# Performance work log

Measured on AMD Instinct MI355X. Metric: run time of the kernel, lower is better.

Reference implementation:

```python
import jax, jax.numpy as jnp
import numpy as np

B, D, L = 16384, 1024, 4


def setup_inputs() -> dict:
    key = jax.random.key(0)
    ks = jax.random.split(key, 5)
    scale = 1.0 / np.sqrt(D)
    x = jax.random.normal(ks[0], (B, D), dtype=jnp.float32)
    # torch nn.Linear default init: U(-1/sqrt(fan_in), 1/sqrt(fan_in))
    Ws = jax.random.uniform(ks[1], (L, D, D), jnp.float32, -scale, scale)
    bs = jax.random.uniform(ks[2], (L, D), jnp.float32, -scale, scale)
    Wo = jax.random.uniform(ks[3], (D, D), jnp.float32, -scale, scale)
    bo = jax.random.uniform(ks[4], (D,), jnp.float32, -scale, scale)
    return {"x": x, "Ws": Ws, "bs": bs, "Wo": Wo, "bo": bo}


def reference(x, Ws, bs, Wo, bo):
    # torch: matmul(x[:, :, None], x[:, None, :]).sum(2) == x * x.sum(-1, keepdims=True)
    interactions = jax.nn.relu(x * jnp.sum(x, axis=-1, keepdims=True))  # (B, D)
    h = x
    for i in range(L):  # fixed small layer count
        h = jax.nn.relu(h @ Ws[i].T + bs[i])  # torch Linear: y = x W^T + b
    out = ((h + interactions) * 0.5) @ Wo.T + bo
    return out
```

## Files before the change

kernel.cpp:

```cpp
#include <hip/hip_runtime.h>


#define DDIM 1024
#define BROWS 16384
#define NIT 8

typedef __attribute__((ext_vector_type(8))) short s8v;
typedef __attribute__((ext_vector_type(4))) float f4v;

__device__ __forceinline__ unsigned short f2bf(float f) {
    unsigned int u = __float_as_uint(f);
    u += 0x7fffu + ((u >> 16) & 1u);
    return (unsigned short)(u >> 16);
}
__device__ __forceinline__ float bf2f(unsigned short u) {
    return __uint_as_float(((unsigned int)u) << 16);
}
__device__ __forceinline__ void gld16(const void* g, void* l) {
    __builtin_amdgcn_global_load_lds(
        (const __attribute__((address_space(1))) unsigned int*)g,
        (__attribute__((address_space(3))) unsigned int*)l, 16, 0, 0);
}

__global__ __launch_bounds__(256) void prep_cvt_kernel(
    const float* __restrict__ x,  const float* __restrict__ Ws,
    const float* __restrict__ Wo, unsigned short* __restrict__ xb,
    unsigned short* __restrict__ wb, float* __restrict__ rowsum)
{
    const int t = threadIdx.x;
    if (blockIdx.x < BROWS) {
        const int row = blockIdx.x;
        const float4 v = *(const float4*)(x + (size_t)row * DDIM + t * 4);
        ushort4 o;
        o.x = f2bf(v.x); o.y = f2bf(v.y); o.z = f2bf(v.z); o.w = f2bf(v.w);
        *(ushort4*)(xb + (size_t)row * DDIM + t * 4) = o;
        float s = v.x + v.y + v.z + v.w;
        #pragma unroll
        for (int off = 32; off > 0; off >>= 1) s += __shfl_down(s, off, 64);
        __shared__ float red[4];
        const int wave = t >> 6, lane = t & 63;
        if (lane == 0) red[wave] = s;
        __syncthreads();
        if (t == 0) rowsum[row] = red[0] + red[1] + red[2] + red[3];
    } else {
        const int base = (blockIdx.x - BROWS) * 1024;
        #pragma unroll
        for (int j = 0; j < 4; ++j) {
            const int idx = base + j * 256 + t;
            const float4 v = (idx < 4 * 262144) ? ((const float4*)Ws)[idx]
                                                : ((const float4*)Wo)[idx - 4 * 262144];
            ushort4 o;
            o.x = f2bf(v.x); o.y = f2bf(v.y); o.z = f2bf(v.z); o.w = f2bf(v.w);
            ((ushort4*)wb)[idx] = o;
        }
    }
}

#define MF(a, b, c) __builtin_amdgcn_mfma_f32_16x16x32_bf16(a, b, c, 0, 0, 0)
#define BAR()   __builtin_amdgcn_s_barrier()
#define VMC(n)  asm volatile("s_waitcnt vmcnt(" #n ")" ::: "memory")

#define SWOFF(lr, cc) ((lr) * 128 + ((((cc) ^ ((lr) & 7))) << 4))

#define SH(src, dst) {                                              \
    gld16((src) + soff,                   (char*)(dst) + t * 16);   \
    gld16((src) + soff + (size_t)64 * K,  (char*)(dst) + t * 16 + 8192); }

#define READ_A(P, m0) {                                                               \
    af[0][0] = *(const s8v*)((const char*)(P) + SWOFF((m0) * 16 + mrow,      quad));      \
    af[0][1] = *(const s8v*)((const char*)(P) + SWOFF((m0) * 16 + mrow,      4 + quad));  \
    af[1][0] = *(const s8v*)((const char*)(P) + SWOFF((m0) * 16 + 16 + mrow, quad));      \
    af[1][1] = *(const s8v*)((const char*)(P) + SWOFF((m0) * 16 + 16 + mrow, 4 + quad)); }

#define READ_B(P) {                                                                   \
    bfr[0][0] = *(const s8v*)((const char*)(P) + SWOFF(bl + mrow,      quad));            \
    bfr[0][1] = *(const s8v*)((const char*)(P) + SWOFF(bl + mrow,      4 + quad));        \
    bfr[1][0] = *(const s8v*)((const char*)(P) + SWOFF(bl + 16 + mrow, quad));            \
    bfr[1][1] = *(const s8v*)((const char*)(P) + SWOFF(bl + 16 + mrow, 4 + quad));        \
    bfr[2][0] = *(const s8v*)((const char*)(P) + SWOFF(bl + 32 + mrow, quad));            \
    bfr[2][1] = *(const s8v*)((const char*)(P) + SWOFF(bl + 32 + mrow, 4 + quad));        \
    bfr[3][0] = *(const s8v*)((const char*)(P) + SWOFF(bl + 48 + mrow, quad));            \
    bfr[3][1] = *(const s8v*)((const char*)(P) + SWOFF(bl + 48 + mrow, 4 + quad)); }

#define MMA8(m0, s) {                                              \
    acc[m0][0]       = MF(af[0][s], bfr[0][s], acc[m0][0]);        \
    acc[m0][1]       = MF(af[0][s], bfr[1][s], acc[m0][1]);        \
    acc[m0][2]       = MF(af[0][s], bfr[2][s], acc[m0][2]);        \
    acc[m0][3]       = MF(af[0][s], bfr[3][s], acc[m0][3]);        \
    acc[(m0) + 1][0] = MF(af[1][s], bfr[0][s], acc[(m0) + 1][0]);  \
    acc[(m0) + 1][1] = MF(af[1][s], bfr[1][s], acc[(m0) + 1][1]);  \
    acc[(m0) + 1][2] = MF(af[1][s], bfr[2][s], acc[(m0) + 1][2]);  \
    acc[(m0) + 1][3] = MF(af[1][s], bfr[3][s], acc[(m0) + 1][3]); }

#define MMA16(m0) { __builtin_amdgcn_s_setprio(1); MMA8(m0, 0) MMA8(m0, 1) \
                    __builtin_amdgcn_s_setprio(0); }

template <int MODE>
__global__ __launch_bounds__(512, 2) void gemm256(
    const unsigned short* __restrict__ A,
    const unsigned short* __restrict__ Bw,
    const float* __restrict__ bias,
    void* __restrict__ out,
    const unsigned short* __restrict__ xb,
    const float* __restrict__ rowsum)
{
    constexpr int K = DDIM, N = DDIM;
    __shared__ unsigned short smem[2][2][2][128 * 64];

    const int t = threadIdx.x;
    const int lane = t & 63;
    const int wid  = t >> 6;
    const int wr   = wid >> 2;
    const int wc   = wid & 3;
    const int mrow = lane & 15;
    const int quad = lane >> 4;
    const int rowBase = blockIdx.x * 256;
    const int colBase = blockIdx.y * 256;

    const unsigned short* const Ab0 = A  + (size_t)rowBase * K;
    const unsigned short* const Ab1 = Ab0 + (size_t)128 * K;
    const unsigned short* const Bb0 = Bw + (size_t)colBase * K;
    const unsigned short* const Bb1 = Bb0 + (size_t)128 * K;

    const int srow = t >> 3;
    const size_t soff = (size_t)srow * K + (size_t)(((t & 7) ^ (srow & 7)) * 8);

    unsigned short* const a00 = &smem[0][0][0][0];
    unsigned short* const a01 = &smem[0][0][1][0];
    unsigned short* const a10 = &smem[0][1][0][0];
    unsigned short* const a11 = &smem[0][1][1][0];
    unsigned short* const b00 = &smem[1][0][0][0];
    unsigned short* const b01 = &smem[1][0][1][0];
    unsigned short* const b10 = &smem[1][1][0][0];
    unsigned short* const b11 = &smem[1][1][1][0];

    const unsigned short* const aR0 = wr ? a01 : a00;
    const unsigned short* const aR1 = wr ? a11 : a10;
    const unsigned short* const bR0 = (wc >> 1) ? b01 : b00;
    const unsigned short* const bR1 = (wc >> 1) ? b11 : b10;
    const int bl = (wc & 1) * 64;

    f4v acc[8][4] = {};
    s8v af[2][2], bfr[4][2];

    SH(Ab0,      a00); SH(Ab1,      a01);
    SH(Bb0,      b00); SH(Bb1,      b01);
    SH(Bb0 + 64, b10); SH(Bb1 + 64, b11);
    VMC(4);
    BAR();
    READ_B(bR0); READ_A(aR0, 0);

    #pragma unroll 1
    for (int it = 0; it < NIT; ++it) {
        const int ka = it * 128, kb = ka + 64;
        const bool more = it < NIT - 1;

        SH(Ab0 + kb, a10);
        BAR(); MMA16(0); BAR();
        READ_A(aR0, 2);
        SH(Ab1 + kb, a11);
        BAR(); MMA16(2); BAR();
        READ_A(aR0, 4);
        if (more) SH(Bb0 + ka + 128, b00);
        BAR(); MMA16(4); BAR();
        READ_A(aR0, 6);
        if (more) SH(Bb1 + ka + 128, b01);
        if (more) { VMC(4); } else { VMC(0); }
        BAR();
        MMA16(6);
        READ_B(bR1); READ_A(aR1, 0);
        BAR();

        if (more) SH(Ab0 + ka + 128, a00);
        BAR(); MMA16(0); BAR();
        READ_A(aR1, 2);
        if (more) SH(Ab1 + ka + 128, a01);
        BAR(); MMA16(2); BAR();
        READ_A(aR1, 4);
        if (more) SH(Bb0 + kb + 128, b10);
        BAR(); MMA16(4); BAR();
        READ_A(aR1, 6);
        if (more) SH(Bb1 + kb + 128, b11);
        if (more) { VMC(4); }
        BAR();
        MMA16(6);
        if (more) { READ_B(bR0); READ_A(aR0, 0); }
        BAR();
    }

    if (MODE == 2) {
        float* sCf = (float*)smem;
        float* o = (float*)out;
        #pragma unroll 1
        for (int half = 0; half < 2; ++half) {
            __syncthreads();
            if (wr == half) {
                #pragma unroll
                for (int ni = 0; ni < 4; ++ni) {
                    const int n = wc * 64 + ni * 16 + mrow;
                    const float bv = bias[colBase + n];
                    #pragma unroll
                    for (int mi = 0; mi < 8; ++mi)
                        #pragma unroll
                        for (int r = 0; r < 4; ++r)
                            sCf[(mi * 16 + quad * 4 + r) * 256 + n] = acc[mi][ni][r] + bv;
                }
            }
            __syncthreads();
            #pragma unroll
            for (int p = 0; p < 16; ++p) {
                const int idx = t + p * 512;
                const int row = idx >> 6, ch = idx & 63;
                const float4 v = ((const float4*)sCf)[idx];
                *(float4*)(o + (size_t)(rowBase + half * 128 + row) * N + colBase + ch * 4) = v;
            }
        }
    } else {
        __syncthreads();
        unsigned short* sC = (unsigned short*)smem;
        #pragma unroll
        for (int ni = 0; ni < 4; ++ni) {
            const int n = wc * 64 + ni * 16 + mrow;
            const float bv = bias[colBase + n];
            #pragma unroll
            for (int mi = 0; mi < 8; ++mi)
                #pragma unroll
                for (int r = 0; r < 4; ++r) {
                    const int row = wr * 128 + mi * 16 + quad * 4 + r;
                    float v = acc[mi][ni][r] + bv;
                    v = v > 0.f ? v : 0.f;
                    sC[row * 256 + n] = f2bf(v);
                }
        }
        __syncthreads();
        unsigned short* o16 = (unsigned short*)out;
        #pragma unroll
        for (int p = 0; p < 16; ++p) {
            const int idx = t + p * 512;
            const int row = idx >> 5, ch = idx & 31;
            s8v c = *(const s8v*)&sC[row * 256 + ch * 8];
            if (MODE == 1) {
                const float rsv = rowsum[rowBase + row];
                const s8v xv = *(const s8v*)&xb[(size_t)(rowBase + row) * DDIM + colBase + ch * 8];
                #pragma unroll
                for (int j = 0; j < 8; ++j) {
                    float itv = bf2f((unsigned short)xv[j]) * rsv;
                    itv = itv > 0.f ? itv : 0.f;
                    c[j] = (short)f2bf(0.5f * (bf2f((unsigned short)c[j]) + itv));
                }
            }
            *(s8v*)&o16[(size_t)(rowBase + row) * DDIM + colBase + ch * 8] = c;
        }
    }
}

extern "C" void kernel_launch(void* const* d_in, const int* in_sizes, int n_in,
                              void* d_out, int out_size, void* d_ws, size_t ws_size,
                              hipStream_t stream) {
    const float* x  = (const float*)d_in[0];
    const float* Ws = (const float*)d_in[1];
    const float* bs = (const float*)d_in[2];
    const float* Wo = (const float*)d_in[3];
    const float* bo = (const float*)d_in[4];
    float* out = (float*)d_out;

    char* ws = (char*)d_ws;
    unsigned short* xb  = (unsigned short*)(ws);
    unsigned short* h0  = (unsigned short*)(ws + 33554432);
    unsigned short* h1  = (unsigned short*)(ws + 67108864);
    unsigned short* wb  = (unsigned short*)(ws + 100663296);
    float*          rsm = (float*)(ws + 111149056);

    prep_cvt_kernel<<<BROWS + 1280, 256, 0, stream>>>(x, Ws, Wo, xb, wb, rsm);

    const size_t WSZ = (size_t)DDIM * DDIM;
    dim3 g(BROWS / 256, DDIM / 256);
    gemm256<0><<<g, 512, 0, stream>>>(xb, wb,           bs,            h0, nullptr, nullptr);
    gemm256<0><<<g, 512, 0, stream>>>(h0, wb + 1 * WSZ, bs + 1 * DDIM, h1, nullptr, nullptr);
    gemm256<0><<<g, 512, 0, stream>>>(h1, wb + 2 * WSZ, bs + 2 * DDIM, h0, nullptr, nullptr);
    gemm256<1><<<g, 512, 0, stream>>>(h0, wb + 3 * WSZ, bs + 3 * DDIM, h1, xb, rsm);
    gemm256<2><<<g, 512, 0, stream>>>(h1, wb + 4 * WSZ, bo,            out, nullptr, nullptr);
}
```

Measured before the change: 317.7 us.

## Fuse prep and all five GEMM layers into one cooperative persistent kernel

Replaces the conversion kernel and the five per-layer GEMM launches with a single cooperative kernel whose 256 blocks each cover one output tile per layer. The input/weight conversion and row sums now run inside it, and grid-wide syncs with thread fences separate the phases. The goal is to remove the launch gaps and tail effects between six kernels. In exchange, every layer waits for the slowest block at a grid barrier, and the cooperative launch requires all 256 blocks to be resident at once (two per CU).

```diff
diff --git a/kernel.cpp b/kernel.cpp
--- a/kernel.cpp
+++ b/kernel.cpp
@@ -1,4 +1,7 @@
 #include <hip/hip_runtime.h>
+#include <hip/hip_cooperative_groups.h>
+
+namespace cg = cooperative_groups;
 
 
 #define DDIM 1024
@@ -20,40 +23,6 @@
     __builtin_amdgcn_global_load_lds(
         (const __attribute__((address_space(1))) unsigned int*)g,
         (__attribute__((address_space(3))) unsigned int*)l, 16, 0, 0);
-}
-
-__global__ __launch_bounds__(256) void prep_cvt_kernel(
-    const float* __restrict__ x,  const float* __restrict__ Ws,
-    const float* __restrict__ Wo, unsigned short* __restrict__ xb,
-    unsigned short* __restrict__ wb, float* __restrict__ rowsum)
-{
-    const int t = threadIdx.x;
-    if (blockIdx.x < BROWS) {
-        const int row = blockIdx.x;
-        const float4 v = *(const float4*)(x + (size_t)row * DDIM + t * 4);
-        ushort4 o;
-        o.x = f2bf(v.x); o.y = f2bf(v.y); o.z = f2bf(v.z); o.w = f2bf(v.w);
-        *(ushort4*)(xb + (size_t)row * DDIM + t * 4) = o;
-        float s = v.x + v.y + v.z + v.w;
-        #pragma unroll
-        for (int off = 32; off > 0; off >>= 1) s += __shfl_down(s, off, 64);
-        __shared__ float red[4];
-        const int wave = t >> 6, lane = t & 63;
-        if (lane == 0) red[wave] = s;
-        __syncthreads();
-        if (t == 0) rowsum[row] = red[0] + red[1] + red[2] + red[3];
-    } else {
-        const int base = (blockIdx.x - BROWS) * 1024;
-        #pragma unroll
-        for (int j = 0; j < 4; ++j) {
-            const int idx = base + j * 256 + t;
-            const float4 v = (idx < 4 * 262144) ? ((const float4*)Ws)[idx]
-                                                : ((const float4*)Wo)[idx - 4 * 262144];
-            ushort4 o;
-            o.x = f2bf(v.x); o.y = f2bf(v.y); o.z = f2bf(v.z); o.w = f2bf(v.w);
-            ((ushort4*)wb)[idx] = o;
-        }
-    }
 }
 
 #define MF(a, b, c) __builtin_amdgcn_mfma_f32_16x16x32_bf16(a, b, c, 0, 0, 0)
@@ -95,17 +64,18 @@
 #define MMA16(m0) { __builtin_amdgcn_s_setprio(1); MMA8(m0, 0) MMA8(m0, 1) \
                     __builtin_amdgcn_s_setprio(0); }
 
-template <int MODE>
-__global__ __launch_bounds__(512, 2) void gemm256(
-    const unsigned short* __restrict__ A,
-    const unsigned short* __restrict__ Bw,
-    const float* __restrict__ bias,
-    void* __restrict__ out,
-    const unsigned short* __restrict__ xb,
-    const float* __restrict__ rowsum)
+__global__ __launch_bounds__(512, 2) void deepfm_fused(
+    const float* __restrict__ x,  const float* __restrict__ Ws,
+    const float* __restrict__ bs, const float* __restrict__ Wo,
+    const float* __restrict__ bo, float* __restrict__ out,
+    unsigned short* __restrict__ xb, unsigned short* __restrict__ h0,
+    unsigned short* __restrict__ h1, unsigned short* __restrict__ wb,
+    float* __restrict__ rsm)
 {
     constexpr int K = DDIM, N = DDIM;
     __shared__ unsigned short smem[2][2][2][128 * 64];
+
+    cg::grid_group grid = cg::this_grid();
 
     const int t = threadIdx.x;
     const int lane = t & 63;
@@ -116,11 +86,40 @@
     const int quad = lane >> 4;
     const int rowBase = blockIdx.x * 256;
     const int colBase = blockIdx.y * 256;
-
-    const unsigned short* const Ab0 = A  + (size_t)rowBase * K;
-    const unsigned short* const Ab1 = Ab0 + (size_t)128 * K;
-    const unsigned short* const Bb0 = Bw + (size_t)colBase * K;
-    const unsigned short* const Bb1 = Bb0 + (size_t)128 * K;
+    const int bid = blockIdx.x * 4 + blockIdx.y;
+
+    {
+        const int rbase = bid * 64;
+        #pragma unroll 1
+        for (int g = 0; g < 8; ++g) {
+            const int row = rbase + g * 8 + wid;
+            const float* xr = x + (size_t)row * DDIM;
+            float s = 0.f;
+            #pragma unroll
+            for (int j = 0; j < 4; ++j) {
+                const float4 v = *(const float4*)(xr + (j * 64 + lane) * 4);
+                ushort4 o;
+                o.x = f2bf(v.x); o.y = f2bf(v.y); o.z = f2bf(v.z); o.w = f2bf(v.w);
+                *(ushort4*)(xb + (size_t)row * DDIM + (j * 64 + lane) * 4) = o;
+                s += v.x + v.y + v.z + v.w;
+            }
+            #pragma unroll
+            for (int off = 32; off > 0; off >>= 1) s += __shfl_down(s, off, 64);
+            if (lane == 0) rsm[row] = s;
+        }
+        #pragma unroll
+        for (int j = 0; j < 10; ++j) {
+            const int idx = bid * 5120 + j * 512 + t;
+            const float4 v = (idx < 4 * 262144) ? ((const float4*)Ws)[idx]
+                                                : ((const float4*)Wo)[idx - 4 * 262144];
+            ushort4 o;
+            o.x = f2bf(v.x); o.y = f2bf(v.y); o.z = f2bf(v.z); o.w = f2bf(v.w);
+            ((ushort4*)wb)[idx] = o;
+        }
+    }
+    __threadfence();
+    grid.sync();
+    __threadfence();
 
     const int srow = t >> 3;
     const size_t soff = (size_t)srow * K + (size_t)(((t & 7) ^ (srow & 7)) * 8);
@@ -140,116 +139,133 @@
     const unsigned short* const bR1 = (wc >> 1) ? b11 : b10;
     const int bl = (wc & 1) * 64;
 
-    f4v acc[8][4] = {};
-    s8v af[2][2], bfr[4][2];
-
-    SH(Ab0,      a00); SH(Ab1,      a01);
-    SH(Bb0,      b00); SH(Bb1,      b01);
-    SH(Bb0 + 64, b10); SH(Bb1 + 64, b11);
-    VMC(4);
-    BAR();
-    READ_B(bR0); READ_A(aR0, 0);
-
     #pragma unroll 1
-    for (int it = 0; it < NIT; ++it) {
-        const int ka = it * 128, kb = ka + 64;
-        const bool more = it < NIT - 1;
-
-        SH(Ab0 + kb, a10);
-        BAR(); MMA16(0); BAR();
-        READ_A(aR0, 2);
-        SH(Ab1 + kb, a11);
-        BAR(); MMA16(2); BAR();
-        READ_A(aR0, 4);
-        if (more) SH(Bb0 + ka + 128, b00);
-        BAR(); MMA16(4); BAR();
-        READ_A(aR0, 6);
-        if (more) SH(Bb1 + ka + 128, b01);
-        if (more) { VMC(4); } else { VMC(0); }
+    for (int l = 0; l < 5; ++l) {
+        const unsigned short* Acur = (l == 0) ? xb : ((l & 1) ? h0 : h1);
+        const unsigned short* Bwc  = wb + (size_t)l * DDIM * DDIM;
+        const float* bias = (l == 4) ? bo : (bs + (size_t)l * DDIM);
+        unsigned short* outb = (l & 1) ? h1 : h0;
+
+        const unsigned short* const Ab0 = Acur + (size_t)rowBase * K;
+        const unsigned short* const Ab1 = Ab0 + (size_t)128 * K;
+        const unsigned short* const Bb0 = Bwc + (size_t)colBase * K;
+        const unsigned short* const Bb1 = Bb0 + (size_t)128 * K;
+
+        f4v acc[8][4] = {};
+        s8v af[2][2], bfr[4][2];
+
+        SH(Ab0,      a00); SH(Ab1,      a01);
+        SH(Bb0,      b00); SH(Bb1,      b01);
+        SH(Bb0 + 64, b10); SH(Bb1 + 64, b11);
+        VMC(4);
         BAR();
-        MMA16(6);
-        READ_B(bR1); READ_A(aR1, 0);
-        BAR();
-
-        if (more) SH(Ab0 + ka + 128, a00);
-        BAR(); MMA16(0); BAR();
-        READ_A(aR1, 2);
-        if (more) SH(Ab1 + ka + 128, a01);
-        BAR(); MMA16(2); BAR();
-        READ_A(aR1, 4);
-        if (more) SH(Bb0 + kb + 128, b10);
-        BAR(); MMA16(4); BAR();
-        READ_A(aR1, 6);
-        if (more) SH(Bb1 + kb + 128, b11);
-        if (more) { VMC(4); }
-        BAR();
-        MMA16(6);
-        if (more) { READ_B(bR0); READ_A(aR0, 0); }
-        BAR();
-    }
-
-    if (MODE == 2) {
-        float* sCf = (float*)smem;
-        float* o = (float*)out;
+        READ_B(bR0); READ_A(aR0, 0);
+
         #pragma unroll 1
-        for (int half = 0; half < 2; ++half) {
+        for (int it = 0; it < NIT; ++it) {
+            const int ka = it * 128, kb = ka + 64;
+            const bool more = it < NIT - 1;
+
+            SH(Ab0 + kb, a10);
+            BAR(); MMA16(0); BAR();
+            READ_A(aR0, 2);
+            SH(Ab1 + kb, a11);
+            BAR(); MMA16(2); BAR();
+            READ_A(aR0, 4);
+            if (more) SH(Bb0 + ka + 128, b00);
+            BAR(); MMA16(4); BAR();
+            READ_A(aR0, 6);
+            if (more) SH(Bb1 + ka + 128, b01);
+            if (more) { VMC(4); } else { VMC(0); }
+            BAR();
+            MMA16(6);
+            READ_B(bR1); READ_A(aR1, 0);
+            BAR();
+
+            if (more) SH(Ab0 + ka + 128, a00);
+            BAR(); MMA16(0); BAR();
+            READ_A(aR1, 2);
+            if (more) SH(Ab1 + ka + 128, a01);
+            BAR(); MMA16(2); BAR();
+            READ_A(aR1, 4);
+            if (more) SH(Bb0 + kb + 128, b10);
+            BAR(); MMA16(4); BAR();
+            READ_A(aR1, 6);
+            if (more) SH(Bb1 + kb + 128, b11);
+            if (more) { VMC(4); }
+            BAR();
+            MMA16(6);
+            if (more) { READ_B(bR0); READ_A(aR0, 0); }
+            BAR();
+        }
+
+        if (l == 4) {
+            float* sCf = (float*)smem;
+            #pragma unroll 1
+            for (int half = 0; half < 2; ++half) {
+                __syncthreads();
+                if (wr == half) {
+                    #pragma unroll
+                    for (int ni = 0; ni < 4; ++ni) {
+                        const int n = wc * 64 + ni * 16 + mrow;
+                        const float bv = bias[colBase + n];
+                        #pragma unroll
+                        for (int mi = 0; mi < 8; ++mi)
+                            #pragma unroll
+                            for (int r = 0; r < 4; ++r)
+                                sCf[(mi * 16 + quad * 4 + r) * 256 + n] = acc[mi][ni][r] + bv;
+                    }
+                }
+                __syncthreads();
+                #pragma unroll
+                for (int p = 0; p < 16; ++p) {
+                    const int idx = t + p * 512;
+                    const int row = idx >> 6, ch = idx & 63;
+                    const float4 v = ((const float4*)sCf)[idx];
+                    *(float4*)(out + (size_t)(rowBase + half * 128 + row) * N + colBase + ch * 4) = v;
+                }
+            }
+        } else {
             __syncthreads();
-            if (wr == half) {
+            unsigned short* sC = (unsigned short*)smem;
+            #pragma unroll
+            for (int ni = 0; ni < 4; ++ni) {
+                const int n = wc * 64 + ni * 16 + mrow;
+                const float bv = bias[colBase + n];
                 #pragma unroll
-                for (int ni = 0; ni < 4; ++ni) {
-                    const int n = wc * 64 + ni * 16 + mrow;
-                    const float bv = bias[colBase + n];
+                for (int mi = 0; mi < 8; ++mi)
                     #pragma unroll
-                    for (int mi = 0; mi < 8; ++mi)
-                        #pragma unroll
-                        for (int r = 0; r < 4; ++r)
-                            sCf[(mi * 16 + quad * 4 + r) * 256 + n] = acc[mi][ni][r] + bv;
-                }
+                    for (int r = 0; r < 4; ++r) {
+                        const int row = wr * 128 + mi * 16 + quad * 4 + r;
+                        float v = acc[mi][ni][r] + bv;
+                        v = v > 0.f ? v : 0.f;
+                        sC[row * 256 + n] = f2bf(v);
+                    }
             }
             __syncthreads();
             #pragma unroll
             for (int p = 0; p < 16; ++p) {
                 const int idx = t + p * 512;
-                const int row = idx >> 6, ch = idx & 63;
-                const float4 v = ((const float4*)sCf)[idx];
-                *(float4*)(o + (size_t)(rowBase + half * 128 + row) * N + colBase + ch * 4) = v;
-            }
-        }
-    } else {
-        __syncthreads();
-        unsigned short* sC = (unsigned short*)smem;
-        #pragma unroll
-        for (int ni = 0; ni < 4; ++ni) {
-            const int n = wc * 64 + ni * 16 + mrow;
-            const float bv = bias[colBase + n];
-            #pragma unroll
-            for (int mi = 0; mi < 8; ++mi)
-                #pragma unroll
-                for (int r = 0; r < 4; ++r) {
-                    const int row = wr * 128 + mi * 16 + quad * 4 + r;
-                    float v = acc[mi][ni][r] + bv;
-                    v = v > 0.f ? v : 0.f;
-                    sC[row * 256 + n] = f2bf(v);
+                const int row = idx >> 5, ch = idx & 31;
+                s8v c = *(const s8v*)&sC[row * 256 + ch * 8];
+                if (l == 3) {
+                    const float rsv = rsm[rowBase + row];
+                    const s8v xv = *(const s8v*)&xb[(size_t)(rowBase + row) * DDIM + colBase + ch * 8];
+                    #pragma unroll
+                    for (int j = 0; j < 8; ++j) {
+                        float itv = bf2f((unsigned short)xv[j]) * rsv;
+                        itv = itv > 0.f ? itv : 0.f;
+                        c[j] = (short)f2bf(0.5f * (bf2f((unsigned short)c[j]) + itv));
+                    }
                 }
-        }
-        __syncthreads();
-        unsigned short* o16 = (unsigned short*)out;
-        #pragma unroll
-        for (int p = 0; p < 16; ++p) {
-            const int idx = t + p * 512;
-            const int row = idx >> 5, ch = idx & 31;
-            s8v c = *(const s8v*)&sC[row * 256 + ch * 8];
-            if (MODE == 1) {
-                const float rsv = rowsum[rowBase + row];
-                const s8v xv = *(const s8v*)&xb[(size_t)(rowBase + row) * DDIM + colBase + ch * 8];
-                #pragma unroll
-                for (int j = 0; j < 8; ++j) {
-                    float itv = bf2f((unsigned short)xv[j]) * rsv;
-                    itv = itv > 0.f ? itv : 0.f;
-                    c[j] = (short)f2bf(0.5f * (bf2f((unsigned short)c[j]) + itv));
-                }
-            }
-            *(s8v*)&o16[(size_t)(rowBase + row) * DDIM + colBase + ch * 8] = c;
+                *(s8v*)&outb[(size_t)(rowBase + row) * DDIM + colBase + ch * 8] = c;
+            }
+        }
+
+        if (l < 4) {
+            __threadfence();
+            grid.sync();
+            __threadfence();
         }
     }
 }
@@ -271,13 +287,9 @@
     unsigned short* wb  = (unsigned short*)(ws + 100663296);
     float*          rsm = (float*)(ws + 111149056);
 
-    prep_cvt_kernel<<<BROWS + 1280, 256, 0, stream>>>(x, Ws, Wo, xb, wb, rsm);
-
-    const size_t WSZ = (size_t)DDIM * DDIM;
-    dim3 g(BROWS / 256, DDIM / 256);
-    gemm256<0><<<g, 512, 0, stream>>>(xb, wb,           bs,            h0, nullptr, nullptr);
-    gemm256<0><<<g, 512, 0, stream>>>(h0, wb + 1 * WSZ, bs + 1 * DDIM, h1, nullptr, nullptr);
-    gemm256<0><<<g, 512, 0, stream>>>(h1, wb + 2 * WSZ, bs + 2 * DDIM, h0, nullptr, nullptr);
-    gemm256<1><<<g, 512, 0, stream>>>(h0, wb + 3 * WSZ, bs + 3 * DDIM, h1, xb, rsm);
-    gemm256<2><<<g, 512, 0, stream>>>(h1, wb + 4 * WSZ, bo,            out, nullptr, nullptr);
-}
+    void* args[11] = {(void*)&x, (void*)&Ws, (void*)&bs, (void*)&Wo, (void*)&bo,
+                      (void*)&out, (void*)&xb, (void*)&h0, (void*)&h1, (void*)&wb,
+                      (void*)&rsm};
+    hipLaunchCooperativeKernel(deepfm_fused, dim3(BROWS / 256, DDIM / 256),
+                               dim3(512), args, 0u, stream);
+}
```

Measured after the change: 923.3 us. +190.6%, slower.
